# Kernel optimization log

Hardware: AMD Instinct MI355X
Metric: run time of the kernel (lower is better)

The kernel has to match this reference:

```python
import jax, jax.numpy as jnp
import numpy as np

B, G, T = 4096, 100, 24


def _greedy_dispatch(demand, caps, prices, slack_price):
    """Exact LP solution of: min prices@alloc + slack_price*slack
    s.t. 0<=alloc<=caps, sum(alloc)+slack = demand (per b,t).
    demand: [B,T] (nonneg), caps: [B,G,T], prices: [G], slack_price: scalar.
    Returns alloc [B,G,T], slack [B,T].
    """
    prices_all = jnp.concatenate([prices, slack_price[None]])        # [G+1]
    # slack capacity = demand itself (slack alone can absorb everything)
    caps_all = jnp.concatenate([caps, demand[:, None, :]], axis=1)    # [B,G+1,T]
    order = jnp.argsort(prices_all)                                   # merit order
    caps_s = caps_all[:, order, :]
    before = jnp.cumsum(caps_s, axis=1) - caps_s                      # capacity ahead in merit order
    alloc_s = jnp.clip(demand[:, None, :] - before, 0.0, caps_s)
    inv = jnp.argsort(order)
    alloc = alloc_s[:, inv, :]
    return alloc[:, :-1, :], alloc[:, -1, :]


def setup_inputs() -> dict:
    key = jax.random.key(0)
    k1, k2, k3, k4 = jax.random.split(key, 4)
    R_up = jax.random.uniform(k1, (B, G, T), dtype=jnp.float32)
    R_dn = jax.random.uniform(k2, (B, G, T), dtype=jnp.float32)
    omega_true = jax.random.normal(k3, (B, T), dtype=jnp.float32) * 5.0
    b_G = 10.0 + 40.0 * jax.random.uniform(k4, (G,), dtype=jnp.float32)  # marginal costs $/MWh
    return {
        "R_up": R_up,
        "R_dn": R_dn,
        "omega_true": omega_true,
        "b_G": b_G,
        "voll": jnp.float32(1000.0),
        "vosp": jnp.float32(500.0),
        "rt_up_ratio": jnp.float32(1.5),
        "rt_dn_ratio": jnp.float32(1.2),
    }


def reference(R_up, R_dn, omega_true, b_G, voll, vosp, rt_up_ratio, rt_dn_ratio):
    c_up = rt_up_ratio * b_G                                          # [G]
    c_dn = rt_dn_ratio * b_G                                          # [G]
    dem_up = jnp.maximum(omega_true, 0.0)                             # [B,T]
    dem_dn = jnp.maximum(-omega_true, 0.0)
    du, LS = _greedy_dispatch(dem_up, R_up, c_up, voll)
    dd, SP = _greedy_dispatch(dem_dn, R_dn, c_dn, vosp)
    rt_obj = (jnp.einsum('g,bgt->b', c_up, du)
              + jnp.einsum('g,bgt->b', c_dn, dd)
              + voll * LS.sum(axis=1) + vosp * SP.sum(axis=1))        # [B]
    return du, dd, LS, SP, rt_obj
```

## Files before the change

### kernel.cpp

```cpp
#include <hip/hip_runtime.h>

#define G_ 100
#define T_ 24
#define GP1 101
#define TILE (G_ * T_)
#define VPB (TILE / 4)
#define BPB 4
#define WPB (BPB * 2)
#define BLOCK (64 * WPB)

typedef float vfloat4 __attribute__((ext_vector_type(4)));

template<int N>
__device__ __forceinline__ void scan_chunk(int k0,
    const float* __restrict__ capp,
    float* __restrict__ gcol,
    int ord_lo, int ord_hi, float pr_lo, float pr_hi,
    float dem, float& before, float& objp)
{
    int gg[N]; float pr[N], cap[N];
#pragma unroll
    for (int j = 0; j < N; ++j) {
        const int idx = k0 + j;
        if (idx < 64) {
            gg[j] = __builtin_amdgcn_readlane(ord_lo, idx);
            pr[j] = __int_as_float(__builtin_amdgcn_readlane(__float_as_int(pr_lo), idx));
        } else {
            gg[j] = __builtin_amdgcn_readlane(ord_hi, idx - 64);
            pr[j] = __int_as_float(__builtin_amdgcn_readlane(__float_as_int(pr_hi), idx - 64));
        }
    }
#pragma unroll
    for (int j = 0; j < N; ++j) cap[j] = capp[gg[j] * T_];
#pragma unroll
    for (int j = 0; j < N; ++j) {
        float a = fminf(fmaxf(dem - before, 0.f), cap[j]);
        before += cap[j];
        objp = fmaf(pr[j], a, objp);
        gcol[gg[j] * T_] = a;
    }
}

__global__ __launch_bounds__(BLOCK, 8) void dispatch_kernel(
    const float* __restrict__ R_up, const float* __restrict__ R_dn,
    const float* __restrict__ omega,
    const float* __restrict__ b_G, const float* __restrict__ voll,
    const float* __restrict__ vosp, const float* __restrict__ ru,
    const float* __restrict__ rd,
    float* __restrict__ out, int B)
{
    __shared__ float s_praw[2][GP1];
    __shared__ int   s_ord [2][128];
    __shared__ float s_pr  [2][128];
    __shared__ float s_obj [WPB];

    const int tid = threadIdx.x;

    if (tid < GP1) {
        float mu, md;
        if (tid < G_) { float bg = b_G[tid]; mu = ru[0] * bg; md = rd[0] * bg; }
        else          { mu = voll[0];        md = vosp[0]; }
        s_praw[0][tid] = mu; s_praw[1][tid] = md;
    }
    __syncthreads();
    {
        const int pass = tid >> 8;
        const int i    = tid & 255;
        if (i < GP1) {
            const float m = s_praw[pass][i];
            int r = 0;
            for (int j = 0; j < GP1; ++j) {
                const float v = s_praw[pass][j];
                r += (v < m) || (v == m && j < i);
            }
            s_ord[pass][r] = i;  s_pr[pass][r] = m;
        }
    }
    __syncthreads();

    const int w    = tid >> 6;
    const int lane = tid & 63;
    const int b = __builtin_amdgcn_readfirstlane(blockIdx.x * BPB + (w >> 1));
    const int p = __builtin_amdgcn_readfirstlane(w & 1);
    const size_t bgt = (size_t)B * TILE;

    const int hi_ok = (lane < GP1 - 64);
    const int   ord_lo = s_ord[p][lane];
    const int   ord_hi = hi_ok ? s_ord[p][64 + lane] : 0;
    const float pr_lo  = s_pr [p][lane];
    const float pr_hi  = hi_ok ? s_pr [p][64 + lane] : 0.f;

    {
        vfloat4* __restrict__ dst = (vfloat4*)out + ((size_t)p * B + b) * VPB;
#pragma unroll
        for (int j = 0; j < 9; ++j) dst[lane + j * 64] = (vfloat4)(0.f);
        if (lane < VPB - 576)       dst[lane + 576]    = (vfloat4)(0.f);
    }
    asm volatile("s_waitcnt vmcnt(0)" ::: "memory");

    const int t = (lane < T_) ? lane : 0;

    float objp = 0.f;
    if (lane < T_) {
        const float om  = omega[(size_t)b * T_ + t];
        const float dem = p ? fmaxf(-om, 0.f) : fmaxf(om, 0.f);
        const float* __restrict__ capp = (p ? R_dn : R_up) + (size_t)b * TILE + t;
        float* __restrict__ gcol = out + (size_t)p * bgt + (size_t)b * TILE + t;

        float before = 0.f;
        scan_chunk<16>( 0, capp, gcol, ord_lo, ord_hi, pr_lo, pr_hi, dem, before, objp);
        bool run = __any(before < dem);
        if (run) { scan_chunk<16>(16, capp, gcol, ord_lo, ord_hi, pr_lo, pr_hi, dem, before, objp);
                   run = __any(before < dem); }
        if (run) { scan_chunk< 8>(32, capp, gcol, ord_lo, ord_hi, pr_lo, pr_hi, dem, before, objp);
                   run = __any(before < dem); }
        if (run) { scan_chunk< 8>(40, capp, gcol, ord_lo, ord_hi, pr_lo, pr_hi, dem, before, objp);
                   run = __any(before < dem); }
        if (run) { scan_chunk< 8>(48, capp, gcol, ord_lo, ord_hi, pr_lo, pr_hi, dem, before, objp);
                   run = __any(before < dem); }
        if (run) { scan_chunk< 8>(56, capp, gcol, ord_lo, ord_hi, pr_lo, pr_hi, dem, before, objp);
                   run = __any(before < dem); }
        if (run) { scan_chunk< 8>(64, capp, gcol, ord_lo, ord_hi, pr_lo, pr_hi, dem, before, objp);
                   run = __any(before < dem); }
        if (run) { scan_chunk< 8>(72, capp, gcol, ord_lo, ord_hi, pr_lo, pr_hi, dem, before, objp);
                   run = __any(before < dem); }
        if (run) { scan_chunk< 8>(80, capp, gcol, ord_lo, ord_hi, pr_lo, pr_hi, dem, before, objp);
                   run = __any(before < dem); }
        if (run) { scan_chunk< 8>(88, capp, gcol, ord_lo, ord_hi, pr_lo, pr_hi, dem, before, objp);
                   run = __any(before < dem); }
        if (run)   scan_chunk< 4>(96, capp, gcol, ord_lo, ord_hi, pr_lo, pr_hi, dem, before, objp);

        const float slack_pr =
            __int_as_float(__builtin_amdgcn_readlane(__float_as_int(pr_hi), GP1 - 1 - 64));
        float slackv = fmaxf(dem - before, 0.f);
        objp = fmaf(slack_pr, slackv, objp);
        out[2 * bgt + (size_t)p * B * T_ + (size_t)b * T_ + t] = slackv;
    }

#pragma unroll
    for (int off = 32; off; off >>= 1) objp += __shfl_xor(objp, off, 64);
    if (lane == 0) s_obj[w] = objp;

    __syncthreads();
    if ((tid & 127) == 0)
        out[2 * bgt + 2 * (size_t)B * T_ + b] = s_obj[w] + s_obj[w + 1];
}

extern "C" void kernel_launch(void* const* d_in, const int* in_sizes, int n_in,
                              void* d_out, int out_size, void* d_ws, size_t ws_size,
                              hipStream_t stream)
{
    const float* R_up  = (const float*)d_in[0];
    const float* R_dn  = (const float*)d_in[1];
    const float* omega = (const float*)d_in[2];
    const float* b_G   = (const float*)d_in[3];
    const float* voll  = (const float*)d_in[4];
    const float* vosp  = (const float*)d_in[5];
    const float* ru    = (const float*)d_in[6];
    const float* rd    = (const float*)d_in[7];

    const int B = in_sizes[0] / TILE;
    float* out = (float*)d_out;

    dispatch_kernel<<<B / BPB, BLOCK, 0, stream>>>(
        R_up, R_dn, omega, b_G, voll, vosp, ru, rd, out, B);
}
```

Measured before the change: 152.8 us.

## Issue zero-fill and omega load before sort; widen first scan chunk

Moves the output zero-fill stores and the omega load ahead of the per-block merit-order sort so that global traffic overlaps the shared-memory ranking work, and merges the price computation into the same thread split. The first scan chunk grows to 48 generators with coarser 16-wide chunks afterward, giving fewer wave-wide early-exit checks and more loads in flight, at the cost of extra scanning when demand is met early. Launch bounds drop from 8 to 6 waves per SIMD so the larger unrolled chunk has room for registers.

Result: slower. 163.0 us (+6.6%).

```diff
diff --git a/kernel.cpp b/kernel.cpp
--- a/kernel.cpp
+++ b/kernel.cpp
@@ -41,7 +41,7 @@
     }
 }
 
-__global__ __launch_bounds__(BLOCK, 8) void dispatch_kernel(
+__global__ __launch_bounds__(BLOCK, 6) void dispatch_kernel(
     const float* __restrict__ R_up, const float* __restrict__ R_dn,
     const float* __restrict__ omega,
     const float* __restrict__ b_G, const float* __restrict__ voll,
@@ -54,35 +54,43 @@
     __shared__ float s_pr  [2][128];
     __shared__ float s_obj [WPB];
 
-    const int tid = threadIdx.x;
-
-    if (tid < GP1) {
-        float mu, md;
-        if (tid < G_) { float bg = b_G[tid]; mu = ru[0] * bg; md = rd[0] * bg; }
-        else          { mu = voll[0];        md = vosp[0]; }
-        s_praw[0][tid] = mu; s_praw[1][tid] = md;
-    }
-    __syncthreads();
-    {
-        const int pass = tid >> 8;
-        const int i    = tid & 255;
-        if (i < GP1) {
-            const float m = s_praw[pass][i];
-            int r = 0;
-            for (int j = 0; j < GP1; ++j) {
-                const float v = s_praw[pass][j];
-                r += (v < m) || (v == m && j < i);
-            }
-            s_ord[pass][r] = i;  s_pr[pass][r] = m;
-        }
-    }
-    __syncthreads();
-
+    const int tid  = threadIdx.x;
     const int w    = tid >> 6;
     const int lane = tid & 63;
     const int b = __builtin_amdgcn_readfirstlane(blockIdx.x * BPB + (w >> 1));
     const int p = __builtin_amdgcn_readfirstlane(w & 1);
     const size_t bgt = (size_t)B * TILE;
+
+    {
+        vfloat4* __restrict__ dst = (vfloat4*)out + ((size_t)p * B + b) * VPB;
+#pragma unroll
+        for (int j = 0; j < 9; ++j) dst[lane + j * 64] = (vfloat4)(0.f);
+        if (lane < VPB - 576)       dst[lane + 576]    = (vfloat4)(0.f);
+    }
+    float om = 0.f;
+    if (lane < T_) om = omega[(size_t)b * T_ + lane];
+
+    {
+        const int sp = tid >> 8;
+        const int si = tid & 255;
+        if (si < GP1) {
+            float m;
+            if (si < G_) m = (sp ? rd[0] : ru[0]) * b_G[si];
+            else         m = sp ? vosp[0] : voll[0];
+            s_praw[sp][si] = m;
+        }
+        __syncthreads();
+        if (si < GP1) {
+            const float m = s_praw[sp][si];
+            int r = 0;
+            for (int j = 0; j < GP1; ++j) {
+                const float v = s_praw[sp][j];
+                r += (v < m) || (v == m && j < si);
+            }
+            s_ord[sp][r] = si;  s_pr[sp][r] = m;
+        }
+    }
+    __syncthreads();
 
     const int hi_ok = (lane < GP1 - 64);
     const int   ord_lo = s_ord[p][lane];
@@ -90,49 +98,29 @@
     const float pr_lo  = s_pr [p][lane];
     const float pr_hi  = hi_ok ? s_pr [p][64 + lane] : 0.f;
 
-    {
-        vfloat4* __restrict__ dst = (vfloat4*)out + ((size_t)p * B + b) * VPB;
-#pragma unroll
-        for (int j = 0; j < 9; ++j) dst[lane + j * 64] = (vfloat4)(0.f);
-        if (lane < VPB - 576)       dst[lane + 576]    = (vfloat4)(0.f);
-    }
     asm volatile("s_waitcnt vmcnt(0)" ::: "memory");
 
     const int t = (lane < T_) ? lane : 0;
-
     float objp = 0.f;
     if (lane < T_) {
-        const float om  = omega[(size_t)b * T_ + t];
         const float dem = p ? fmaxf(-om, 0.f) : fmaxf(om, 0.f);
         const float* __restrict__ capp = (p ? R_dn : R_up) + (size_t)b * TILE + t;
         float* __restrict__ gcol = out + (size_t)p * bgt + (size_t)b * TILE + t;
 
         float before = 0.f;
-        scan_chunk<16>( 0, capp, gcol, ord_lo, ord_hi, pr_lo, pr_hi, dem, before, objp);
+        scan_chunk<48>( 0, capp, gcol, ord_lo, ord_hi, pr_lo, pr_hi, dem, before, objp);
         bool run = __any(before < dem);
-        if (run) { scan_chunk<16>(16, capp, gcol, ord_lo, ord_hi, pr_lo, pr_hi, dem, before, objp);
+        if (run) { scan_chunk<16>(48, capp, gcol, ord_lo, ord_hi, pr_lo, pr_hi, dem, before, objp);
                    run = __any(before < dem); }
-        if (run) { scan_chunk< 8>(32, capp, gcol, ord_lo, ord_hi, pr_lo, pr_hi, dem, before, objp);
+        if (run) { scan_chunk<16>(64, capp, gcol, ord_lo, ord_hi, pr_lo, pr_hi, dem, before, objp);
                    run = __any(before < dem); }
-        if (run) { scan_chunk< 8>(40, capp, gcol, ord_lo, ord_hi, pr_lo, pr_hi, dem, before, objp);
-                   run = __any(before < dem); }
-        if (run) { scan_chunk< 8>(48, capp, gcol, ord_lo, ord_hi, pr_lo, pr_hi, dem, before, objp);
-                   run = __any(before < dem); }
-        if (run) { scan_chunk< 8>(56, capp, gcol, ord_lo, ord_hi, pr_lo, pr_hi, dem, before, objp);
-                   run = __any(before < dem); }
-        if (run) { scan_chunk< 8>(64, capp, gcol, ord_lo, ord_hi, pr_lo, pr_hi, dem, before, objp);
-                   run = __any(before < dem); }
-        if (run) { scan_chunk< 8>(72, capp, gcol, ord_lo, ord_hi, pr_lo, pr_hi, dem, before, objp);
-                   run = __any(before < dem); }
-        if (run) { scan_chunk< 8>(80, capp, gcol, ord_lo, ord_hi, pr_lo, pr_hi, dem, before, objp);
-                   run = __any(before < dem); }
-        if (run) { scan_chunk< 8>(88, capp, gcol, ord_lo, ord_hi, pr_lo, pr_hi, dem, before, objp);
+        if (run) { scan_chunk<16>(80, capp, gcol, ord_lo, ord_hi, pr_lo, pr_hi, dem, before, objp);
                    run = __any(before < dem); }
         if (run)   scan_chunk< 4>(96, capp, gcol, ord_lo, ord_hi, pr_lo, pr_hi, dem, before, objp);
 
         const float slack_pr =
             __int_as_float(__builtin_amdgcn_readlane(__float_as_int(pr_hi), GP1 - 1 - 64));
-        float slackv = fmaxf(dem - before, 0.f);
+        const float slackv = fmaxf(dem - before, 0.f);
         objp = fmaf(slack_pr, slackv, objp);
         out[2 * bgt + (size_t)p * B * T_ + (size_t)b * T_ + t] = slackv;
     }
```
